# Kernel optimization log

Measured on AMD Instinct MI355X. Metric: run time of the kernel, lower is better.

The kernel has to match this reference:

```python
import jax, jax.numpy as jnp
import numpy as np

BN_EPS = 1e-5
RMS_EPS = 1e-6
LA_EPS = 0.0005


def _conv_bn(x, w, gamma, beta):
    """1x1 conv (no bias) + BatchNorm2d with batch stats (training mode)."""
    y = jnp.einsum('oc,bchw->bohw', w, x)
    mean = y.mean(axis=(0, 2, 3), keepdims=True)
    var = y.var(axis=(0, 2, 3), keepdims=True)
    return gamma[None, :, None, None] * (y - mean) * jax.lax.rsqrt(var + BN_EPS) + beta[None, :, None, None]


def setup_inputs() -> dict:
    key = jax.random.key(0)
    k0, k1, k2 = jax.random.split(key, 3)
    dim, d = 512, 512  # d = make_divisible(dim / attn_reduce, 8) with attn_reduce=1
    x = jax.random.normal(k0, (8, dim, 64, 64), jnp.float32)
    qkvg_w = jax.random.normal(k1, (4 * d, dim), jnp.float32) * (dim ** -0.5)
    qkvg_gamma = jnp.ones((4 * d,), jnp.float32)
    qkvg_beta = jnp.zeros((4 * d,), jnp.float32)
    attn_norm_w = jnp.ones((d,), jnp.float32)
    proj_w = jax.random.normal(k2, (dim, d), jnp.float32) * (d ** -0.5)
    proj_gamma = jnp.ones((dim,), jnp.float32)
    proj_beta = jnp.zeros((dim,), jnp.float32)
    return {"x": x, "qkvg_w": qkvg_w, "qkvg_gamma": qkvg_gamma, "qkvg_beta": qkvg_beta,
            "attn_norm_w": attn_norm_w, "proj_w": proj_w, "proj_gamma": proj_gamma,
            "proj_beta": proj_beta}


def reference(x, qkvg_w, qkvg_gamma, qkvg_beta, attn_norm_w, proj_w, proj_gamma, proj_beta):
    B, C, H, W = x.shape
    y = _conv_bn(x, qkvg_w, qkvg_gamma, qkvg_beta).reshape(B, -1, H * W)  # (B, 4d, N)
    q, k, v, g = jnp.split(y, 4, axis=1)  # each (B, d, N)

    # LA branch: kernel feature map + linear-associativity (use_linear True since N > d)
    q = jax.nn.sigmoid(q)
    k = jax.nn.sigmoid(k)
    n = q.shape[-1]
    scale = n ** -0.5  # kT.shape[-2] ** -0.5
    # z = kT.mean(-2, keepdims) @ q + eps  -> (B, 1, N), computed on UNscaled k
    z = jnp.einsum('bd,bdn->bn', k.mean(axis=-1), q)[:, None, :] + LA_EPS
    # attn = (v*s) @ (kT*s) @ q ; contract over N first: (B,d,d), then over d
    vk = jnp.einsum('bdn,ben->bde', v * scale, k * scale)  # (B, d, d)
    attn = jnp.einsum('bde,ben->bdn', vk, q) / z  # (B, d, N)

    # RMSNorm over channel dim d
    o = attn * jax.lax.rsqrt(jnp.mean(attn * attn, axis=1, keepdims=True) + RMS_EPS)
    o = o * attn_norm_w[None, :, None]

    # gate + output projection
    o = o * jax.nn.silu(g)
    o = o.reshape(B, -1, H, W)
    return _conv_bn(o, proj_w, proj_gamma, proj_beta)
```

## Files before the change

kernel.cpp:

```cpp
#include <hip/hip_runtime.h>
#include <hip/hip_bf16.h>
#include <math.h>

typedef unsigned short u16;
typedef __attribute__((ext_vector_type(8))) short frag8;
typedef __attribute__((ext_vector_type(4))) float f32x4;
typedef __attribute__((ext_vector_type(8))) unsigned short us8;
typedef __attribute__((ext_vector_type(4))) unsigned short us4;

#define B_ 8
#define C_ 512
#define D_ 512
#define N_ 4096

__device__ __forceinline__ float b2f(u16 u){ union { unsigned int i; float f; } v; v.i = ((unsigned int)u) << 16; return v.f; }
__device__ __forceinline__ u16 f2b(float f){ union { float f; unsigned int i; } v; v.f = f; unsigned int x = v.i; return (u16)((x + 0x7fffu + ((x >> 16) & 1u)) >> 16); }
__device__ __forceinline__ float sigm(float x){ return 1.0f / (1.0f + __expf(-x)); }

__device__ __forceinline__ void gl2l(const u16* g, u16* l){
    __builtin_amdgcn_global_load_lds((const __attribute__((address_space(1))) void*)g,
                                     (__attribute__((address_space(3))) void*)l, 16, 0, 0);
}

__device__ __forceinline__ us8 load_x8(const void* __restrict__ x, int fl, size_t off){
    if (fl){
        const float* p = (const float*)x + off;
        f32x4 a = *(const f32x4*)p;
        f32x4 b = *(const f32x4*)(p + 4);
        us8 o;
        #pragma unroll
        for (int j = 0; j < 4; ++j){ o[j] = f2b(a[j]); o[4 + j] = f2b(b[j]); }
        return o;
    }
    return *(const us8*)((const u16*)x + off);
}

__global__ __launch_bounds__(256) void k_detect(const unsigned int* __restrict__ x, int* __restrict__ flag){
    int tid = threadIdx.x;
    unsigned int w = x[tid];
    int e = (int)((w >> 7) & 0xFFu);
    int in = (e >= 100 && e <= 140) ? 1 : 0;
    __shared__ int sm[4];
    for (int off = 32; off > 0; off >>= 1) in += __shfl_down(in, off);
    if ((tid & 63) == 0) sm[tid >> 6] = in;
    __syncthreads();
    if (tid == 0) *flag = ((sm[0] + sm[1] + sm[2] + sm[3]) < 128) ? 1 : 0;
}

__global__ __launch_bounds__(256) void k_convert(const void* __restrict__ src, u16* __restrict__ dst,
                                                 int n, const int* __restrict__ flag){
    int i = (blockIdx.x * 256 + threadIdx.x) * 8;
    if (i >= n) return;
    *(us8*)(dst + i) = load_x8(src, *flag, (size_t)i);
}

__global__ __launch_bounds__(256) void k_prep(const void* __restrict__ x, const int* __restrict__ flag,
                                              u16* __restrict__ xc, u16* __restrict__ xT, float* __restrict__ mx){
    __shared__ __attribute__((aligned(16))) u16 T[64][72];
    int rt = blockIdx.y;
    int b = rt >> 3, c0 = (rt & 7) * 64;
    int n0 = blockIdx.x * 64;
    int tid = threadIdx.x, fl = *flag;
    int row = tid >> 2, cg = (tid & 3) * 16;
    size_t base = ((size_t)b * C_ + c0 + row) * N_ + n0 + cg;
    us8 v0 = load_x8(x, fl, base);
    us8 v1 = load_x8(x, fl, base + 8);
    u16* xcd = xc + base;
    *(us8*)xcd = v0;
    *(us8*)(xcd + 8) = v1;
    float s = 0.f;
    #pragma unroll
    for (int j = 0; j < 8; ++j) s += b2f(v0[j]) + b2f(v1[j]);
    s += __shfl_xor(s, 1);
    s += __shfl_xor(s, 2);
    if ((tid & 3) == 0) atomicAdd(&mx[c0 + row], s * (1.0f / 32768.0f));
    #pragma unroll
    for (int j = 0; j < 8; ++j){ T[cg + j][row] = v0[j]; T[cg + 8 + j][row] = v1[j]; }
    __syncthreads();
    int col = tid >> 2, rg = (tid & 3) * 16;
    us8 o0 = *(const us8*)&T[col][rg];
    us8 o1 = *(const us8*)&T[col][rg + 8];
    u16* dst = xT + ((size_t)b * N_ + n0 + col) * C_ + c0 + rg;
    *(us8*)dst = o0;
    *(us8*)(dst + 8) = o1;
}

__global__ __launch_bounds__(256) void k_gram_split(const u16* __restrict__ xc, float* __restrict__ Gf){
    __shared__ __attribute__((aligned(16))) u16 As[128 * 32];
    __shared__ __attribute__((aligned(16))) u16 Bs[128 * 32];
    int k0 = blockIdx.y * 128, kp0 = blockIdx.x * 128;
    int s = blockIdx.z;
    int b = s >> 2, nbase = (s & 3) * 1024;
    int tid = threadIdx.x, w = tid >> 6, l = tid & 63, lr = l & 15, q = l >> 4;
    int wr = w & 1, wcn = w >> 1;
    int srow = l >> 2, scol = (l & 3) * 8;
    const u16* ap = xc + ((size_t)b * C_ + k0 + w * 16 + srow) * N_ + nbase + scol;
    const u16* bp = xc + ((size_t)b * C_ + kp0 + w * 16 + srow) * N_ + nbase + scol;
    u16* la = As + w * 512;
    u16* lb = Bs + w * 512;
    f32x4 acc[4][4] = {};
    for (int n0 = 0; n0 < 1024; n0 += 32){
        gl2l(ap + n0, la);
        gl2l(ap + n0 + (size_t)64 * N_, la + 2048);
        gl2l(bp + n0, lb);
        gl2l(bp + n0 + (size_t)64 * N_, lb + 2048);
        __syncthreads();
        frag8 af[4], bf[4];
        #pragma unroll
        for (int i = 0; i < 4; ++i){
            af[i] = *(const frag8*)&As[(wr * 64 + i * 16 + lr) * 32 + q * 8];
            bf[i] = *(const frag8*)&Bs[(wcn * 64 + i * 16 + lr) * 32 + q * 8];
        }
        #pragma unroll
        for (int mi = 0; mi < 4; ++mi)
            #pragma unroll
            for (int ni = 0; ni < 4; ++ni)
                acc[mi][ni] = __builtin_amdgcn_mfma_f32_16x16x32_bf16(af[mi], bf[ni], acc[mi][ni], 0, 0, 0);
        __syncthreads();
    }
    #pragma unroll
    for (int mi = 0; mi < 4; ++mi)
        #pragma unroll
        for (int ni = 0; ni < 4; ++ni)
            #pragma unroll
            for (int r = 0; r < 4; ++r)
                atomicAdd(&Gf[(size_t)(k0 + wr * 64 + mi * 16 + q * 4 + r) * C_ + kp0 + wcn * 64 + ni * 16 + lr],
                          acc[mi][ni][r]);
}

__global__ __launch_bounds__(256) void k_gram_fin(const float* __restrict__ Gf, u16* __restrict__ Gb){
    int i = blockIdx.x * 256 + threadIdx.x;
    Gb[i] = f2b(Gf[i] * (1.0f / 32768.0f));
}

__global__ __launch_bounds__(256) void k_wg(const u16* __restrict__ wc, const u16* __restrict__ Gb, float* __restrict__ T){
    __shared__ __attribute__((aligned(16))) u16 As[64][40];
    __shared__ __attribute__((aligned(16))) u16 Bs[64][40];
    int o0 = blockIdx.y * 64, kp0 = blockIdx.x * 64;
    int tid = threadIdx.x, row = tid >> 2, cg = (tid & 3) * 8;
    const u16* ap = wc + (size_t)(o0 + row) * C_ + cg;
    const u16* bp = Gb + (size_t)(kp0 + row) * C_ + cg;
    int w = tid >> 6, l = tid & 63, lr = l & 15, q = l >> 4;
    f32x4 acc[4] = {};
    for (int k0 = 0; k0 < 512; k0 += 32){
        *(us8*)&As[row][cg] = *(const us8*)(ap + k0);
        *(us8*)&Bs[row][cg] = *(const us8*)(bp + k0);
        __syncthreads();
        frag8 af = *(const frag8*)&As[w * 16 + lr][q * 8];
        #pragma unroll
        for (int t4 = 0; t4 < 4; ++t4){
            frag8 bfv = *(const frag8*)&Bs[t4 * 16 + lr][q * 8];
            acc[t4] = __builtin_amdgcn_mfma_f32_16x16x32_bf16(af, bfv, acc[t4], 0, 0, 0);
        }
        __syncthreads();
    }
    #pragma unroll
    for (int t4 = 0; t4 < 4; ++t4)
        #pragma unroll
        for (int r = 0; r < 4; ++r)
            T[(size_t)(o0 + w * 16 + q * 4 + r) * C_ + kp0 + t4 * 16 + lr] = acc[t4][r];
}

__global__ __launch_bounds__(256) void k_bn1fin(const float* __restrict__ T, const u16* __restrict__ wc,
                                                const float* __restrict__ mx, const u16* __restrict__ g1,
                                                const u16* __restrict__ b1, float* __restrict__ s1,
                                                float* __restrict__ t1){
    int o = blockIdx.x, tid = threadIdx.x;
    float e2 = 0.f, mn = 0.f;
    for (int k = tid; k < 512; k += 256){
        float wv = b2f(wc[(size_t)o * C_ + k]);
        e2 += T[(size_t)o * C_ + k] * wv;
        mn += wv * mx[k];
    }
    __shared__ float sm[8];
    for (int off = 32; off > 0; off >>= 1){ e2 += __shfl_down(e2, off); mn += __shfl_down(mn, off); }
    int w = tid >> 6;
    if ((tid & 63) == 0){ sm[w] = e2; sm[4 + w] = mn; }
    __syncthreads();
    if (tid == 0){
        float E2 = sm[0] + sm[1] + sm[2] + sm[3];
        float M  = sm[4] + sm[5] + sm[6] + sm[7];
        float var = E2 - M * M;
        float inv = rsqrtf(var + 1e-5f);
        float sc = b2f(g1[o]) * inv;
        s1[o] = sc;
        t1[o] = b2f(b1[o]) - M * sc;
    }
}

template<int PHASE>
__global__ __launch_bounds__(256) void k_gemm_act(const u16* __restrict__ wc, const u16* __restrict__ xT,
                                                  const float* __restrict__ s1, const float* __restrict__ t1,
                                                  u16* __restrict__ dst){
    __shared__ __attribute__((aligned(16))) u16 As[128 * 32];
    __shared__ __attribute__((aligned(16))) u16 Bs[128 * 32];
    int b = blockIdx.z, n0 = blockIdx.x * 128, my = blockIdx.y;
    int c0 = (PHASE == 1) ? (512 + my * 128) : ((my < 4) ? my * 128 : 1536 + (my - 4) * 128);
    int tid = threadIdx.x, w = tid >> 6, l = tid & 63, lr = l & 15, q = l >> 4;
    int wr = w & 1, wcn = w >> 1;
    int srow = l >> 2, scol = (l & 3) * 8;
    const u16* ap = wc + (size_t)(c0 + w * 16 + srow) * C_ + scol;
    const u16* bp = xT + ((size_t)b * N_ + n0 + w * 16 + srow) * C_ + scol;
    u16* la = As + w * 512;
    u16* lb = Bs + w * 512;
    f32x4 acc[4][4] = {};
    for (int k0 = 0; k0 < 512; k0 += 32){
        gl2l(ap + k0, la);
        gl2l(ap + k0 + (size_t)64 * C_, la + 2048);
        gl2l(bp + k0, lb);
        gl2l(bp + k0 + (size_t)64 * C_, lb + 2048);
        __syncthreads();
        frag8 af[4], bf[4];
        #pragma unroll
        for (int i = 0; i < 4; ++i){
            af[i] = *(const frag8*)&As[(wr * 64 + i * 16 + lr) * 32 + q * 8];
            bf[i] = *(const frag8*)&Bs[(wcn * 64 + i * 16 + lr) * 32 + q * 8];
        }
        #pragma unroll
        for (int mi = 0; mi < 4; ++mi)
            #pragma unroll
            for (int ni = 0; ni < 4; ++ni)
                acc[mi][ni] = __builtin_amdgcn_mfma_f32_16x16x32_bf16(af[mi], bf[ni], acc[mi][ni], 0, 0, 0);
        __syncthreads();
    }
    #pragma unroll
    for (int mi = 0; mi < 4; ++mi){
        int cb = c0 + wr * 64 + mi * 16 + q * 4;
        #pragma unroll
        for (int ni = 0; ni < 4; ++ni){
            int n = n0 + wcn * 64 + ni * 16 + lr;
            us4 o4;
            #pragma unroll
            for (int r = 0; r < 4; ++r){
                int c = cb + r;
                float ybn = acc[mi][ni][r] * s1[c] + t1[c];
                float ov = (c < 1024) ? sigm(ybn) : ((c < 1536) ? ybn : ybn * sigm(ybn));
                if (PHASE == 1)
                    dst[((size_t)b * 1024 + (c - 512)) * N_ + n] = f2b(ov);
                else
                    o4[r] = f2b(ov);
            }
            if (PHASE == 2){
                int col = (cb < 512) ? cb : (cb - 1024);
                *(us4*)(dst + ((size_t)b * N_ + n) * 1024 + col) = o4;
            }
        }
    }
}

__global__ __launch_bounds__(256) void k_vk(const u16* __restrict__ kv, u16* __restrict__ vk){
    __shared__ __attribute__((aligned(16))) u16 As[64 * 32];
    __shared__ __attribute__((aligned(16))) u16 Bs[128 * 32];
    int b = blockIdx.z, d0 = blockIdx.y * 64, e0 = blockIdx.x * 128;
    int tid = threadIdx.x, w = tid >> 6, l = tid & 63, lr = l & 15, q = l >> 4;
    int wr = w & 1, wcn = w >> 1;
    int srow = l >> 2, scol = (l & 3) * 8;
    const u16* ap = kv + ((size_t)b * 1024 + 512 + d0 + w * 16 + srow) * N_ + scol;
    const u16* bp = kv + ((size_t)b * 1024 + e0 + w * 32 + srow) * N_ + scol;
    u16* la = As + w * 512;
    u16* lb = Bs + w * 1024;
    f32x4 acc[2][4] = {};
    for (int n0 = 0; n0 < N_; n0 += 32){
        gl2l(ap + n0, la);
        gl2l(bp + n0, lb);
        gl2l(bp + n0 + (size_t)16 * N_, lb + 512);
        __syncthreads();
        frag8 af[2], bf[4];
        #pragma unroll
        for (int i = 0; i < 2; ++i)
            af[i] = *(const frag8*)&As[(wr * 32 + i * 16 + lr) * 32 + q * 8];
        #pragma unroll
        for (int i = 0; i < 4; ++i)
            bf[i] = *(const frag8*)&Bs[(wcn * 64 + i * 16 + lr) * 32 + q * 8];
        #pragma unroll
        for (int mi = 0; mi < 2; ++mi)
            #pragma unroll
            for (int ni = 0; ni < 4; ++ni)
                acc[mi][ni] = __builtin_amdgcn_mfma_f32_16x16x32_bf16(af[mi], bf[ni], acc[mi][ni], 0, 0, 0);
        __syncthreads();
    }
    #pragma unroll
    for (int mi = 0; mi < 2; ++mi)
        #pragma unroll
        for (int ni = 0; ni < 4; ++ni)
            #pragma unroll
            for (int r = 0; r < 4; ++r)
                vk[((size_t)b * D_ + d0 + wr * 32 + mi * 16 + q * 4 + r) * D_ + e0 + wcn * 64 + ni * 16 + lr]
                    = f2b(acc[mi][ni][r] * (1.0f / 4096.0f));
}

__global__ __launch_bounds__(256) void k_kmean(const u16* __restrict__ kv, u16* __restrict__ kmean){
    int b = blockIdx.y, d = blockIdx.x, tid = threadIdx.x;
    const u16* p = kv + ((size_t)b * 1024 + d) * N_;
    float sum = 0.f;
    for (int i = tid * 8; i < N_; i += 2048){
        us8 v = *(const us8*)(p + i);
        #pragma unroll
        for (int j = 0; j < 8; ++j) sum += b2f(v[j]);
    }
    __shared__ float sm[4];
    for (int off = 32; off > 0; off >>= 1) sum += __shfl_down(sum, off);
    if ((tid & 63) == 0) sm[tid >> 6] = sum;
    __syncthreads();
    if (tid == 0) kmean[b * D_ + d] = f2b((sm[0] + sm[1] + sm[2] + sm[3]) * (1.0f / 4096.0f));
}

__global__ __launch_bounds__(256) void k_attn(const u16* __restrict__ qg, const u16* __restrict__ vk,
                                              const u16* __restrict__ kmean, const u16* __restrict__ anw,
                                              u16* __restrict__ og){
    __shared__ __attribute__((aligned(16))) u16 Xls[32][520];
    __shared__ float sred[4][32];
    int b = blockIdx.y, n0 = blockIdx.x * 32, tid = threadIdx.x;
    int wv = tid >> 6, l = tid & 63, lr = l & 15, q = l >> 4;
    const u16* qb = qg + ((size_t)b * N_ + n0) * 1024;
    #pragma unroll
    for (int it = 0; it < 8; ++it){
        int g = it * 256 + tid;
        int row = g >> 6, col = (g & 63) * 8;
        *(us8*)&Xls[row][col] = *(const us8*)(qb + (size_t)row * 1024 + col);
    }
    __syncthreads();
    const u16* vkb = vk + (size_t)b * D_ * D_ + (size_t)(wv * 128) * D_;
    const u16* kmb = kmean + (size_t)b * D_;
    f32x4 acc[8][2] = {};
    f32x4 accz[2] = {};
    for (int e0 = 0; e0 < 512; e0 += 32){
        frag8 bfv[2];
        #pragma unroll
        for (int nn = 0; nn < 2; ++nn)
            bfv[nn] = *(const frag8*)&Xls[nn * 16 + lr][e0 + q * 8];
        frag8 zf = {};
        if (lr == 0) zf = *(const frag8*)(kmb + e0 + q * 8);
        #pragma unroll
        for (int nn = 0; nn < 2; ++nn)
            accz[nn] = __builtin_amdgcn_mfma_f32_16x16x32_bf16(zf, bfv[nn], accz[nn], 0, 0, 0);
        #pragma unroll
        for (int dd = 0; dd < 8; ++dd){
            frag8 af = *(const frag8*)(vkb + (size_t)(dd * 16 + lr) * D_ + e0 + q * 8);
            #pragma unroll
            for (int nn = 0; nn < 2; ++nn)
                acc[dd][nn] = __builtin_amdgcn_mfma_f32_16x16x32_bf16(af, bfv[nn], acc[dd][nn], 0, 0, 0);
        }
    }
    float rz[2];
    #pragma unroll
    for (int nn = 0; nn < 2; ++nn)
        rz[nn] = 1.0f / (__shfl(accz[nn][0], lr) + 0.0005f);
    float ssq[2] = {0.f, 0.f};
    #pragma unroll
    for (int dd = 0; dd < 8; ++dd)
        #pragma unroll
        for (int nn = 0; nn < 2; ++nn)
            #pragma unroll
            for (int r = 0; r < 4; ++r){
                float a = acc[dd][nn][r] * rz[nn];
                acc[dd][nn][r] = a;
                ssq[nn] += a * a;
            }
    #pragma unroll
    for (int nn = 0; nn < 2; ++nn){
        ssq[nn] += __shfl_xor(ssq[nn], 16);
        ssq[nn] += __shfl_xor(ssq[nn], 32);
    }
    if (l < 16){ sred[wv][l] = ssq[0]; sred[wv][16 + l] = ssq[1]; }
    __syncthreads();
    float rinv[2];
    #pragma unroll
    for (int nn = 0; nn < 2; ++nn){
        float t = sred[0][nn * 16 + lr] + sred[1][nn * 16 + lr] + sred[2][nn * 16 + lr] + sred[3][nn * 16 + lr];
        rinv[nn] = rsqrtf(t * (1.0f / 512.0f) + 1e-6f);
    }
    #pragma unroll
    for (int dd = 0; dd < 8; ++dd){
        int dbase = wv * 128 + dd * 16 + q * 4;
        us4 aw4 = *(const us4*)(anw + dbase);
        #pragma unroll
        for (int nn = 0; nn < 2; ++nn){
            int n = n0 + nn * 16 + lr;
            us4 g4 = *(const us4*)(qb + (size_t)(nn * 16 + lr) * 1024 + 512 + dbase);
            us4 o4;
            #pragma unroll
            for (int r = 0; r < 4; ++r)
                o4[r] = f2b(acc[dd][nn][r] * rinv[nn] * b2f(aw4[r]) * b2f(g4[r]));
            *(us4*)(og + ((size_t)b * N_ + n) * D_ + dbase) = o4;
        }
    }
}

__global__ __launch_bounds__(256) void k_proj(const u16* __restrict__ P, const u16* __restrict__ og, float* __restrict__ po){
    __shared__ __attribute__((aligned(16))) u16 As[128 * 32];
    __shared__ __attribute__((aligned(16))) u16 Bs[128 * 32];
    int b = blockIdx.z, n0 = blockIdx.x * 128, c0 = blockIdx.y * 128;
    int tid = threadIdx.x, w = tid >> 6, l = tid & 63, lr = l & 15, q = l >> 4;
    int wr = w & 1, wcn = w >> 1;
    int srow = l >> 2, scol = (l & 3) * 8;
    const u16* ap = P + (size_t)(c0 + w * 16 + srow) * D_ + scol;
    const u16* bp = og + ((size_t)b * N_ + n0 + w * 16 + srow) * D_ + scol;
    u16* la = As + w * 512;
    u16* lb = Bs + w * 512;
    f32x4 acc[4][4] = {};
    for (int k0 = 0; k0 < 512; k0 += 32){
        gl2l(ap + k0, la);
        gl2l(ap + k0 + (size_t)64 * D_, la + 2048);
        gl2l(bp + k0, lb);
        gl2l(bp + k0 + (size_t)64 * D_, lb + 2048);
        __syncthreads();
        frag8 af[4], bf[4];
        #pragma unroll
        for (int i = 0; i < 4; ++i){
            af[i] = *(const frag8*)&As[(wr * 64 + i * 16 + lr) * 32 + q * 8];
            bf[i] = *(const frag8*)&Bs[(wcn * 64 + i * 16 + lr) * 32 + q * 8];
        }
        #pragma unroll
        for (int mi = 0; mi < 4; ++mi)
            #pragma unroll
            for (int ni = 0; ni < 4; ++ni)
                acc[mi][ni] = __builtin_amdgcn_mfma_f32_16x16x32_bf16(af[mi], bf[ni], acc[mi][ni], 0, 0, 0);
        __syncthreads();
    }
    #pragma unroll
    for (int mi = 0; mi < 4; ++mi){
        int cb = c0 + wr * 64 + mi * 16 + q * 4;
        #pragma unroll
        for (int ni = 0; ni < 4; ++ni){
            int n = n0 + wcn * 64 + ni * 16 + lr;
            #pragma unroll
            for (int r = 0; r < 4; ++r)
                po[((size_t)b * C_ + cb + r) * N_ + n] = acc[mi][ni][r];
        }
    }
}

__global__ __launch_bounds__(256) void k_bnstats(const float* __restrict__ y, const u16* __restrict__ gamma,
                                                 const u16* __restrict__ beta, float* __restrict__ s,
                                                 float* __restrict__ t){
    int ch = blockIdx.x, tid = threadIdx.x;
    float sum = 0.f, ss = 0.f;
    for (int b = 0; b < B_; ++b){
        const float* p = y + ((size_t)b * C_ + ch) * N_;
        for (int i = tid * 4; i < N_; i += 1024){
            f32x4 v = *(const f32x4*)(p + i);
            #pragma unroll
            for (int j = 0; j < 4; ++j){ sum += v[j]; ss += v[j] * v[j]; }
        }
    }
    __shared__ float sm[8];
    for (int off = 32; off > 0; off >>= 1){ sum += __shfl_down(sum, off); ss += __shfl_down(ss, off); }
    int w = tid >> 6;
    if ((tid & 63) == 0){ sm[w] = sum; sm[4 + w] = ss; }
    __syncthreads();
    if (tid == 0){
        float S = sm[0] + sm[1] + sm[2] + sm[3];
        float Q = sm[4] + sm[5] + sm[6] + sm[7];
        float mean = S / 32768.f;
        float var = Q / 32768.f - mean * mean;
        float inv = rsqrtf(var + 1e-5f);
        float sc = b2f(gamma[ch]) * inv;
        s[ch] = sc;
        t[ch] = b2f(beta[ch]) - mean * sc;
    }
}

__global__ __launch_bounds__(256) void k_bnapply(float* __restrict__ po, const float* __restrict__ s,
                                                 const float* __restrict__ t){
    size_t idx = ((size_t)blockIdx.x * 256 + threadIdx.x) * 8;
    int c = (int)((idx >> 12) & 511);
    float sc = s[c], tc = t[c];
    f32x4 a = *(const f32x4*)(po + idx);
    f32x4 b = *(const f32x4*)(po + idx + 4);
    #pragma unroll
    for (int j = 0; j < 4; ++j){ a[j] = a[j] * sc + tc; b[j] = b[j] * sc + tc; }
    *(f32x4*)(po + idx) = a;
    *(f32x4*)(po + idx + 4) = b;
}

extern "C" void kernel_launch(void* const* d_in, const int* in_sizes, int n_in,
                              void* d_out, int out_size, void* d_ws, size_t ws_size,
                              hipStream_t stream){
    float* out = (float*)d_out;
    char* ws = (char*)d_ws;

    int*   flag  = (int*)ws;
    float* s1    = (float*)(ws + 4096);
    float* t1    = (float*)(ws + 12288);
    float* s2    = (float*)(ws + 20480);
    float* t2    = (float*)(ws + 22528);
    float* mx    = (float*)(ws + 24576);
    u16*   kmean = (u16*)(ws + 28672);
    u16*   g1c   = (u16*)(ws + 36864);
    u16*   b1c   = (u16*)(ws + 40960);
    u16*   anwc  = (u16*)(ws + 45056);
    u16*   g2c   = (u16*)(ws + 46080);
    u16*   b2c   = (u16*)(ws + 47104);
    u16*   wc    = (u16*)(ws + (1ull << 20));
    u16*   pc    = (u16*)(ws + (3ull << 20));
    u16*   Gb    = (u16*)(ws + (3584ull << 10));
    float* T     = (float*)(ws + (4ull << 20));
    u16*   vkall = (u16*)(ws + (8ull << 20));
    u16*   kv    = (u16*)(ws + (12ull << 20));
    u16*   xc    = (u16*)(ws + (12ull << 20));
    u16*   og    = (u16*)(ws + (76ull << 20));
    u16*   xT    = (u16*)(ws + (76ull << 20));
    float* Gf    = (float*)(ws + (108ull << 20));

    k_detect<<<1, 256, 0, stream>>>((const unsigned int*)d_in[0], flag);
    k_convert<<<512, 256, 0, stream>>>(d_in[1], wc, 1048576, flag);
    k_convert<<<1, 256, 0, stream>>>(d_in[2], g1c, 2048, flag);
    k_convert<<<1, 256, 0, stream>>>(d_in[3], b1c, 2048, flag);
    k_convert<<<1, 256, 0, stream>>>(d_in[4], anwc, 512, flag);
    k_convert<<<128, 256, 0, stream>>>(d_in[5], pc, 262144, flag);
    k_convert<<<1, 256, 0, stream>>>(d_in[6], g2c, 512, flag);
    k_convert<<<1, 256, 0, stream>>>(d_in[7], b2c, 512, flag);

    hipMemsetAsync(mx, 0, C_ * sizeof(float), stream);
    hipMemsetAsync(Gf, 0, C_ * C_ * sizeof(float), stream);
    k_prep<<<dim3(64, 64), 256, 0, stream>>>(d_in[0], flag, xc, xT, mx);

    k_gram_split<<<dim3(4, 4, 32), 256, 0, stream>>>(xc, Gf);
    k_gram_fin<<<1024, 256, 0, stream>>>(Gf, Gb);
    k_wg<<<dim3(8, 32), 256, 0, stream>>>(wc, Gb, T);
    k_bn1fin<<<2048, 256, 0, stream>>>(T, wc, mx, g1c, b1c, s1, t1);

    k_gemm_act<1><<<dim3(32, 8, 8), 256, 0, stream>>>(wc, xT, s1, t1, kv);
    k_vk<<<dim3(4, 8, 8), 256, 0, stream>>>(kv, vkall);
    k_kmean<<<dim3(512, 8), 256, 0, stream>>>(kv, kmean);

    k_gemm_act<2><<<dim3(32, 8, 8), 256, 0, stream>>>(wc, xT, s1, t1, kv);
    k_attn<<<dim3(128, 8), 256, 0, stream>>>(kv, vkall, kmean, anwc, og);

    k_proj<<<dim3(32, 4, 8), 256, 0, stream>>>(pc, og, out);
    k_bnstats<<<512, 256, 0, stream>>>(out, g2c, b2c, s2, t2);
    k_bnapply<<<8192, 256, 0, stream>>>(out, s2, t2);
}
```

Baseline: 563.3 us.

## Fuse output BN statistics into projection GEMM epilogue and widen attention blocks

The projection GEMM now reduces per-channel sums and sums of squares in its epilogue and accumulates them with atomics. A tiny finalize kernel then computes the scale and shift, which removes the separate pass that reread the 64MB fp32 output for BN statistics. Separately, the attention kernel runs 512 threads (8 waves) per block, each wave owning 64 output channels instead of 128. This lowers per-wave accumulator registers and adds parallelism. The fused statistics use float atomics, so summation order becomes nondeterministic, and the extra waves duplicate the z-computation MFMAs.

```diff
diff --git a/kernel.cpp b/kernel.cpp
--- a/kernel.cpp
+++ b/kernel.cpp
@@ -305,24 +305,24 @@
     if (tid == 0) kmean[b * D_ + d] = f2b((sm[0] + sm[1] + sm[2] + sm[3]) * (1.0f / 4096.0f));
 }
 
-__global__ __launch_bounds__(256) void k_attn(const u16* __restrict__ qg, const u16* __restrict__ vk,
+__global__ __launch_bounds__(512) void k_attn(const u16* __restrict__ qg, const u16* __restrict__ vk,
                                               const u16* __restrict__ kmean, const u16* __restrict__ anw,
                                               u16* __restrict__ og){
     __shared__ __attribute__((aligned(16))) u16 Xls[32][520];
-    __shared__ float sred[4][32];
+    __shared__ float sred[8][32];
     int b = blockIdx.y, n0 = blockIdx.x * 32, tid = threadIdx.x;
     int wv = tid >> 6, l = tid & 63, lr = l & 15, q = l >> 4;
     const u16* qb = qg + ((size_t)b * N_ + n0) * 1024;
     #pragma unroll
-    for (int it = 0; it < 8; ++it){
-        int g = it * 256 + tid;
+    for (int it = 0; it < 4; ++it){
+        int g = it * 512 + tid;
         int row = g >> 6, col = (g & 63) * 8;
         *(us8*)&Xls[row][col] = *(const us8*)(qb + (size_t)row * 1024 + col);
     }
     __syncthreads();
-    const u16* vkb = vk + (size_t)b * D_ * D_ + (size_t)(wv * 128) * D_;
+    const u16* vkb = vk + (size_t)b * D_ * D_ + (size_t)(wv * 64) * D_;
     const u16* kmb = kmean + (size_t)b * D_;
-    f32x4 acc[8][2] = {};
+    f32x4 acc[4][2] = {};
     f32x4 accz[2] = {};
     for (int e0 = 0; e0 < 512; e0 += 32){
         frag8 bfv[2];
@@ -335,7 +335,7 @@
         for (int nn = 0; nn < 2; ++nn)
             accz[nn] = __builtin_amdgcn_mfma_f32_16x16x32_bf16(zf, bfv[nn], accz[nn], 0, 0, 0);
         #pragma unroll
-        for (int dd = 0; dd < 8; ++dd){
+        for (int dd = 0; dd < 4; ++dd){
             frag8 af = *(const frag8*)(vkb + (size_t)(dd * 16 + lr) * D_ + e0 + q * 8);
             #pragma unroll
             for (int nn = 0; nn < 2; ++nn)
@@ -348,7 +348,7 @@
         rz[nn] = 1.0f / (__shfl(accz[nn][0], lr) + 0.0005f);
     float ssq[2] = {0.f, 0.f};
     #pragma unroll
-    for (int dd = 0; dd < 8; ++dd)
+    for (int dd = 0; dd < 4; ++dd)
         #pragma unroll
         for (int nn = 0; nn < 2; ++nn)
             #pragma unroll
@@ -367,12 +367,14 @@
     float rinv[2];
     #pragma unroll
     for (int nn = 0; nn < 2; ++nn){
-        float t = sred[0][nn * 16 + lr] + sred[1][nn * 16 + lr] + sred[2][nn * 16 + lr] + sred[3][nn * 16 + lr];
+        float t = 0.f;
+        #pragma unroll
+        for (int wi = 0; wi < 8; ++wi) t += sred[wi][nn * 16 + lr];
         rinv[nn] = rsqrtf(t * (1.0f / 512.0f) + 1e-6f);
     }
     #pragma unroll
-    for (int dd = 0; dd < 8; ++dd){
-        int dbase = wv * 128 + dd * 16 + q * 4;
+    for (int dd = 0; dd < 4; ++dd){
+        int dbase = wv * 64 + dd * 16 + q * 4;
         us4 aw4 = *(const us4*)(anw + dbase);
         #pragma unroll
         for (int nn = 0; nn < 2; ++nn){
@@ -387,7 +389,8 @@
     }
 }
 
-__global__ __launch_bounds__(256) void k_proj(const u16* __restrict__ P, const u16* __restrict__ og, float* __restrict__ po){
+__global__ __launch_bounds__(256) void k_proj(const u16* __restrict__ P, const u16* __restrict__ og, float* __restrict__ po,
+                                              float* __restrict__ bns, float* __restrict__ bnq){
     __shared__ __attribute__((aligned(16))) u16 As[128 * 32];
     __shared__ __attribute__((aligned(16))) u16 Bs[128 * 32];
     int b = blockIdx.z, n0 = blockIdx.x * 128, c0 = blockIdx.y * 128;
@@ -428,37 +431,33 @@
             for (int r = 0; r < 4; ++r)
                 po[((size_t)b * C_ + cb + r) * N_ + n] = acc[mi][ni][r];
         }
-    }
-}
-
-__global__ __launch_bounds__(256) void k_bnstats(const float* __restrict__ y, const u16* __restrict__ gamma,
-                                                 const u16* __restrict__ beta, float* __restrict__ s,
-                                                 float* __restrict__ t){
-    int ch = blockIdx.x, tid = threadIdx.x;
-    float sum = 0.f, ss = 0.f;
-    for (int b = 0; b < B_; ++b){
-        const float* p = y + ((size_t)b * C_ + ch) * N_;
-        for (int i = tid * 4; i < N_; i += 1024){
-            f32x4 v = *(const f32x4*)(p + i);
-            #pragma unroll
-            for (int j = 0; j < 4; ++j){ sum += v[j]; ss += v[j] * v[j]; }
-        }
-    }
-    __shared__ float sm[8];
-    for (int off = 32; off > 0; off >>= 1){ sum += __shfl_down(sum, off); ss += __shfl_down(ss, off); }
-    int w = tid >> 6;
-    if ((tid & 63) == 0){ sm[w] = sum; sm[4 + w] = ss; }
-    __syncthreads();
-    if (tid == 0){
-        float S = sm[0] + sm[1] + sm[2] + sm[3];
-        float Q = sm[4] + sm[5] + sm[6] + sm[7];
-        float mean = S / 32768.f;
-        float var = Q / 32768.f - mean * mean;
-        float inv = rsqrtf(var + 1e-5f);
-        float sc = b2f(gamma[ch]) * inv;
-        s[ch] = sc;
-        t[ch] = b2f(beta[ch]) - mean * sc;
-    }
+        #pragma unroll
+        for (int r = 0; r < 4; ++r){
+            float s = 0.f, ss = 0.f;
+            #pragma unroll
+            for (int ni = 0; ni < 4; ++ni){ float v = acc[mi][ni][r]; s += v; ss += v * v; }
+            s += __shfl_xor(s, 1);  ss += __shfl_xor(ss, 1);
+            s += __shfl_xor(s, 2);  ss += __shfl_xor(ss, 2);
+            s += __shfl_xor(s, 4);  ss += __shfl_xor(ss, 4);
+            s += __shfl_xor(s, 8);  ss += __shfl_xor(ss, 8);
+            if (lr == 0){
+                atomicAdd(&bns[cb + r], s);
+                atomicAdd(&bnq[cb + r], ss);
+            }
+        }
+    }
+}
+
+__global__ __launch_bounds__(256) void k_bn2fin(const float* __restrict__ bns, const float* __restrict__ bnq,
+                                                const u16* __restrict__ gamma, const u16* __restrict__ beta,
+                                                float* __restrict__ s, float* __restrict__ t){
+    int c = blockIdx.x * 256 + threadIdx.x;
+    float mean = bns[c] * (1.0f / 32768.0f);
+    float var = bnq[c] * (1.0f / 32768.0f) - mean * mean;
+    float inv = rsqrtf(var + 1e-5f);
+    float sc = b2f(gamma[c]) * inv;
+    s[c] = sc;
+    t[c] = b2f(beta[c]) - mean * sc;
 }
 
 __global__ __launch_bounds__(256) void k_bnapply(float* __restrict__ po, const float* __restrict__ s,
@@ -492,6 +491,8 @@
     u16*   anwc  = (u16*)(ws + 45056);
     u16*   g2c   = (u16*)(ws + 46080);
     u16*   b2c   = (u16*)(ws + 47104);
+    float* bns   = (float*)(ws + 53248);
+    float* bnq   = (float*)(ws + 57344);
     u16*   wc    = (u16*)(ws + (1ull << 20));
     u16*   pc    = (u16*)(ws + (3ull << 20));
     u16*   Gb    = (u16*)(ws + (3584ull << 10));
@@ -514,6 +515,8 @@
 
     hipMemsetAsync(mx, 0, C_ * sizeof(float), stream);
     hipMemsetAsync(Gf, 0, C_ * C_ * sizeof(float), stream);
+    hipMemsetAsync(bns, 0, C_ * sizeof(float), stream);
+    hipMemsetAsync(bnq, 0, C_ * sizeof(float), stream);
     k_prep<<<dim3(64, 64), 256, 0, stream>>>(d_in[0], flag, xc, xT, mx);
 
     k_gram_split<<<dim3(4, 4, 32), 256, 0, stream>>>(xc, Gf);
@@ -526,9 +529,9 @@
     k_kmean<<<dim3(512, 8), 256, 0, stream>>>(kv, kmean);
 
     k_gemm_act<2><<<dim3(32, 8, 8), 256, 0, stream>>>(wc, xT, s1, t1, kv);
-    k_attn<<<dim3(128, 8), 256, 0, stream>>>(kv, vkall, kmean, anwc, og);
-
-    k_proj<<<dim3(32, 4, 8), 256, 0, stream>>>(pc, og, out);
-    k_bnstats<<<512, 256, 0, stream>>>(out, g2c, b2c, s2, t2);
+    k_attn<<<dim3(128, 8), 512, 0, stream>>>(kv, vkall, kmean, anwc, og);
+
+    k_proj<<<dim3(32, 4, 8), 256, 0, stream>>>(pc, og, out, bns, bnq);
+    k_bn2fin<<<2, 256, 0, stream>>>(bns, bnq, g2c, b2c, s2, t2);
     k_bnapply<<<8192, 256, 0, stream>>>(out, s2, t2);
 }
```

Measured after the change: 589.8 us. +4.7%, slower.
